# Optimization experiments

Measured on AMD Instinct MI355X. Metric: run time of the kernel, lower is better.

## Reference

```python
import jax, jax.numpy as jnp
import numpy as np

B, T, E = 8, 2048, 512   # batch, tokens, embedding_dim
K, C = 8192, 8           # num_embeddings, codebook_dim
LN_EPS = 1e-5


def _layer_norm(x, g, b):
    mu = jnp.mean(x, axis=-1, keepdims=True)
    var = jnp.var(x, axis=-1, keepdims=True)
    return (x - mu) * jax.lax.rsqrt(var + LN_EPS) * g + b


def setup_inputs() -> dict:
    key = jax.random.key(0)
    ks = jax.random.split(key, 8)
    s_e = 1.0 / np.sqrt(E)
    s_c = 1.0 / np.sqrt(C)
    return {
        "features": jax.random.normal(ks[0], (B, T, E), dtype=jnp.float32),
        # project_in: Linear(E,E) -> ReLU -> Linear(E,C)
        "W1_in": jax.random.uniform(ks[1], (E, E), jnp.float32, -s_e, s_e),
        "b1_in": jnp.zeros((E,), jnp.float32),
        "W2_in": jax.random.uniform(ks[2], (E, C), jnp.float32, -s_e, s_e),
        "b2_in": jnp.zeros((C,), jnp.float32),
        "ln_in_g": jnp.ones((C,), jnp.float32),
        "ln_in_b": jnp.zeros((C,), jnp.float32),
        # codebook
        "emb": jax.random.normal(ks[3], (K, C), dtype=jnp.float32),
        # project_out: Linear(C,E) -> ReLU -> Linear(E,E)
        "W1_out": jax.random.uniform(ks[4], (C, E), jnp.float32, -s_c, s_c),
        "b1_out": jnp.zeros((E,), jnp.float32),
        "W2_out": jax.random.uniform(ks[5], (E, E), jnp.float32, -s_e, s_e),
        "b2_out": jnp.zeros((E,), jnp.float32),
        "ln_out_g": jnp.ones((E,), jnp.float32),
        "ln_out_b": jnp.zeros((E,), jnp.float32),
    }


def reference(features, W1_in, b1_in, W2_in, b2_in, ln_in_g, ln_in_b, emb,
              W1_out, b1_out, W2_out, b2_out, ln_out_g, ln_out_b):
    # project_in + norm_in
    h = jax.nn.relu(jnp.einsum('bte,ef->btf', features, W1_in) + b1_in)
    z = jnp.einsum('bte,ec->btc', h, W2_in) + b2_in          # (B,T,C)
    z = _layer_norm(z, ln_in_g, ln_in_b)
    zf = z.reshape(-1, C)                                     # (N,C)
    d = (jnp.sum(zf * zf, axis=1, keepdims=True)
         - 2.0 * zf @ emb.T
         + jnp.sum(emb * emb, axis=1)[None, :])               # (N,K)
    idx = jnp.argmin(d, axis=1)                               # (N,)
    encodings = jax.nn.one_hot(idx, K, dtype=zf.dtype)        # (N,K)
    quantized = emb[idx]                                      # gather == one_hot @ emb
    # project_out + norm_out
    q = jax.nn.relu(quantized @ W1_out + b1_out)
    q = q @ W2_out + b2_out
    q = _layer_norm(q, ln_out_g, ln_out_b)
    q = q.reshape(B, T, E)
    return q, idx[:, None], encodings
```

## Files before the change

### kernel.cpp

```cpp
#include <hip/hip_runtime.h>
#include <cstdint>
#include <cstddef>

#define N_TOK 16384
#define E_DIM 512
#define C_DIM 8
#define K_CODES 8192
#define LN_EPS 1e-5f

typedef __attribute__((ext_vector_type(8))) short short8;
typedef __attribute__((ext_vector_type(4))) float f32x4;

__device__ __forceinline__ unsigned short bf16_rn(float x) {
  unsigned u = __float_as_uint(x);
  unsigned r = u + 0x7FFFu + ((u >> 16) & 1u);
  return (unsigned short)(r >> 16);
}
__device__ __forceinline__ float bf16_f(unsigned short h) {
  return __uint_as_float(((unsigned)h) << 16);
}

__device__ __forceinline__ void gload16(const void* g, void* l) {
  __builtin_amdgcn_global_load_lds(
      (const __attribute__((address_space(1))) void*)g,
      (__attribute__((address_space(3))) void*)l, 16, 0, 0);
}

__device__ __forceinline__ void pack_a_body(const float* __restrict__ A,
    unsigned short* __restrict__ hi, unsigned short* __restrict__ lo, int t) {
  int l = t & 63;
  int kt = (t >> 6) & 15;
  int mf = t >> 10;
  const float* src = A + (size_t)(mf * 16 + (l & 15)) * 512 + kt * 32 + (l >> 4) * 8;
  float4 x0 = *(const float4*)src;
  float4 x1 = *(const float4*)(src + 4);
  float xs[8] = {x0.x, x0.y, x0.z, x0.w, x1.x, x1.y, x1.z, x1.w};
  unsigned hw[4], lw[4];
#pragma unroll
  for (int p = 0; p < 4; ++p) {
    float a = xs[2 * p], b = xs[2 * p + 1];
    unsigned short ha = bf16_rn(a), hb = bf16_rn(b);
    unsigned short la = bf16_rn(a - bf16_f(ha)), lb = bf16_rn(b - bf16_f(hb));
    hw[p] = (unsigned)ha | ((unsigned)hb << 16);
    lw[p] = (unsigned)la | ((unsigned)lb << 16);
  }
  uint4 hv; hv.x = hw[0]; hv.y = hw[1]; hv.z = hw[2]; hv.w = hw[3];
  uint4 lv; lv.x = lw[0]; lv.y = lw[1]; lv.z = lw[2]; lv.w = lw[3];
  ((uint4*)hi)[t] = hv;
  ((uint4*)lo)[t] = lv;
}

__device__ __forceinline__ void pack_b_body(const float* __restrict__ B,
    unsigned short* __restrict__ hi, unsigned short* __restrict__ lo, int t) {
  int l = t & 63;
  int kt = (t >> 6) & 15;
  int nf = t >> 10;
  int col = nf * 16 + (l & 15);
  int krow = kt * 32 + (l >> 4) * 8;
  unsigned hw[4], lw[4];
#pragma unroll
  for (int p = 0; p < 4; ++p) {
    float a = B[(size_t)(krow + 2 * p) * 512 + col];
    float b = B[(size_t)(krow + 2 * p + 1) * 512 + col];
    unsigned short ha = bf16_rn(a), hb = bf16_rn(b);
    unsigned short la = bf16_rn(a - bf16_f(ha)), lb = bf16_rn(b - bf16_f(hb));
    hw[p] = (unsigned)ha | ((unsigned)hb << 16);
    lw[p] = (unsigned)la | ((unsigned)lb << 16);
  }
  uint4 hv; hv.x = hw[0]; hv.y = hw[1]; hv.z = hw[2]; hv.w = hw[3];
  uint4 lv; lv.x = lw[0]; lv.y = lw[1]; lv.z = lw[2]; lv.w = lw[3];
  ((uint4*)hi)[t] = hv;
  ((uint4*)lo)[t] = lv;
}

__global__ __launch_bounds__(256) void prep(const float* __restrict__ features,
    const float* __restrict__ W1_in, const float* __restrict__ W2_out,
    const float* __restrict__ emb,
    const float* __restrict__ W1_out, const float* __restrict__ b1_out,
    unsigned short* __restrict__ A1h, unsigned short* __restrict__ A1l,
    unsigned short* __restrict__ B1h, unsigned short* __restrict__ B1l,
    unsigned short* __restrict__ B2h, unsigned short* __restrict__ B2l,
    unsigned short* __restrict__ A2h, unsigned short* __restrict__ A2l,
    float* __restrict__ ne) {
  int bid = blockIdx.x;
  int tid = threadIdx.x;
  if (bid < 4096) {
    pack_a_body(features, A1h, A1l, bid * 256 + tid);
  } else if (bid < 4224) {
    pack_b_body(W1_in, B1h, B1l, (bid - 4096) * 256 + tid);
  } else if (bid < 4352) {
    pack_b_body(W2_out, B2h, B2l, (bid - 4224) * 256 + tid);
  } else if (bid < 4384) {
    int k = (bid - 4352) * 256 + tid;
    const float* e = emb + (size_t)k * C_DIM;
    float s = 0.f;
#pragma unroll
    for (int c = 0; c < C_DIM; ++c) s = fmaf(e[c], e[c], s);
    ne[k] = s;
  } else {
    int mf = bid - 4384;
    int l = tid & 63;
    int kt4 = tid >> 6;
    int k0 = mf * 16 + (l & 15);
    float ev[C_DIM];
#pragma unroll
    for (int c = 0; c < C_DIM; ++c) ev[c] = emb[(size_t)k0 * C_DIM + c];
#pragma unroll
    for (int it = 0; it < 4; ++it) {
      int kt = it * 4 + kt4;
      int e0 = kt * 32 + (l >> 4) * 8;
      float o[8];
      float4 bv0 = *(const float4*)(b1_out + e0);
      float4 bv1 = *(const float4*)(b1_out + e0 + 4);
      o[0] = bv0.x; o[1] = bv0.y; o[2] = bv0.z; o[3] = bv0.w;
      o[4] = bv1.x; o[5] = bv1.y; o[6] = bv1.z; o[7] = bv1.w;
#pragma unroll
      for (int c = 0; c < C_DIM; ++c) {
        float4 w0 = *(const float4*)(W1_out + (size_t)c * E_DIM + e0);
        float4 w1 = *(const float4*)(W1_out + (size_t)c * E_DIM + e0 + 4);
        o[0] = fmaf(ev[c], w0.x, o[0]); o[1] = fmaf(ev[c], w0.y, o[1]);
        o[2] = fmaf(ev[c], w0.z, o[2]); o[3] = fmaf(ev[c], w0.w, o[3]);
        o[4] = fmaf(ev[c], w1.x, o[4]); o[5] = fmaf(ev[c], w1.y, o[5]);
        o[6] = fmaf(ev[c], w1.z, o[6]); o[7] = fmaf(ev[c], w1.w, o[7]);
      }
      unsigned hw[4], lw[4];
#pragma unroll
      for (int p = 0; p < 4; ++p) {
        float a = fmaxf(o[2 * p], 0.f), b = fmaxf(o[2 * p + 1], 0.f);
        unsigned short ha = bf16_rn(a), hb = bf16_rn(b);
        unsigned short la = bf16_rn(a - bf16_f(ha)), lb = bf16_rn(b - bf16_f(hb));
        hw[p] = (unsigned)ha | ((unsigned)hb << 16);
        lw[p] = (unsigned)la | ((unsigned)lb << 16);
      }
      size_t t = ((size_t)mf * 16 + kt) * 64 + l;
      uint4 hv; hv.x = hw[0]; hv.y = hw[1]; hv.z = hw[2]; hv.w = hw[3];
      uint4 lv; lv.x = lw[0]; lv.y = lw[1]; lv.z = lw[2]; lv.w = lw[3];
      ((uint4*)A2h)[t] = hv;
      ((uint4*)A2l)[t] = lv;
    }
  }
}

template<bool RELU>
__global__ __launch_bounds__(256) void gemm_mfma(const unsigned short* __restrict__ Ah,
    const unsigned short* __restrict__ Al, const unsigned short* __restrict__ Bh,
    const unsigned short* __restrict__ Bl, const float* __restrict__ bias,
    float* __restrict__ C) {
  __shared__ char smem[65536];
  const int tid = threadIdx.x;
  const int l = tid & 63;
  const int w = tid >> 6;
  const int wm = w >> 1, wn = w & 1;
  const int mblk = blockIdx.y, nblk = blockIdx.x;

  const char* gAh = (const char*)Ah + (((size_t)(mblk * 8 + 2 * w) * 16) * 64 + l) * 16;
  const char* gAl = (const char*)Al + (((size_t)(mblk * 8 + 2 * w) * 16) * 64 + l) * 16;
  const char* gBh = (const char*)Bh + (((size_t)(nblk * 8 + 2 * w) * 16) * 64 + l) * 16;
  const char* gBl = (const char*)Bl + (((size_t)(nblk * 8 + 2 * w) * 16) * 64 + l) * 16;

  f32x4 acc[4][4];
#pragma unroll
  for (int i = 0; i < 4; ++i)
#pragma unroll
    for (int j = 0; j < 4; ++j) acc[i][j] = (f32x4){0.f, 0.f, 0.f, 0.f};

  auto stage = [&](int buf, int kt) {
    char* base = smem + buf * 32768;
    const size_t ko = (size_t)kt * 1024;
    char* dA0 = base + (2 * w) * 1024;
    char* dA1 = base + 8192 + (2 * w) * 1024;
    char* dB0 = base + 16384 + (2 * w) * 1024;
    char* dB1 = base + 24576 + (2 * w) * 1024;
    gload16(gAh + ko,         dA0);
    gload16(gAh + ko + 16384, dA0 + 1024);
    gload16(gAl + ko,         dA1);
    gload16(gAl + ko + 16384, dA1 + 1024);
    gload16(gBh + ko,         dB0);
    gload16(gBh + ko + 16384, dB0 + 1024);
    gload16(gBl + ko,         dB1);
    gload16(gBl + ko + 16384, dB1 + 1024);
  };

  auto compute = [&](int buf) {
    const char* base = smem + buf * 32768;
    const short8* sAh = (const short8*)(base);
    const short8* sAl = (const short8*)(base + 8192);
    const short8* sBh = (const short8*)(base + 16384);
    const short8* sBl = (const short8*)(base + 24576);
    short8 a_h[4], a_l[4], b_h[4], b_l[4];
#pragma unroll
    for (int i = 0; i < 4; ++i) {
      a_h[i] = sAh[(wm * 4 + i) * 64 + l];
      a_l[i] = sAl[(wm * 4 + i) * 64 + l];
    }
#pragma unroll
    for (int j = 0; j < 4; ++j) {
      b_h[j] = sBh[(wn * 4 + j) * 64 + l];
      b_l[j] = sBl[(wn * 4 + j) * 64 + l];
    }
#pragma unroll
    for (int i = 0; i < 4; ++i)
#pragma unroll
      for (int j = 0; j < 4; ++j)
        acc[i][j] = __builtin_amdgcn_mfma_f32_16x16x32_bf16(a_h[i], b_h[j], acc[i][j], 0, 0, 0);
#pragma unroll
    for (int i = 0; i < 4; ++i)
#pragma unroll
      for (int j = 0; j < 4; ++j)
        acc[i][j] = __builtin_amdgcn_mfma_f32_16x16x32_bf16(a_h[i], b_l[j], acc[i][j], 0, 0, 0);
#pragma unroll
    for (int i = 0; i < 4; ++i)
#pragma unroll
      for (int j = 0; j < 4; ++j)
        acc[i][j] = __builtin_amdgcn_mfma_f32_16x16x32_bf16(a_l[i], b_h[j], acc[i][j], 0, 0, 0);
  };

  stage(0, 0);
  __syncthreads();
  int cur = 0;
#pragma unroll 1
  for (int kt = 1; kt < 16; ++kt) {
    stage(cur ^ 1, kt);
    compute(cur);
    __syncthreads();
    cur ^= 1;
  }
  compute(cur);

  const int colb = nblk * 128 + wn * 64 + (l & 15);
  const int rowb = mblk * 128 + wm * 64 + ((l >> 4) << 2);
#pragma unroll
  for (int j = 0; j < 4; ++j) {
    float bv = bias[colb + j * 16];
#pragma unroll
    for (int i = 0; i < 4; ++i) {
#pragma unroll
      for (int r = 0; r < 4; ++r) {
        float v = acc[i][j][r] + bv;
        if (RELU) v = fmaxf(v, 0.f);
        C[(size_t)(rowb + i * 16 + r) * 512 + colb + j * 16] = v;
      }
    }
  }
}

__global__ __launch_bounds__(256) void zln_kernel(const float* __restrict__ h,
    const float* __restrict__ W2, const float* __restrict__ b2,
    const float* __restrict__ g, const float* __restrict__ b,
    float* __restrict__ z) {
  int token = blockIdx.x * 4 + (threadIdx.x >> 6);
  int lane = threadIdx.x & 63;
  const float* hr = h + (size_t)token * E_DIM;
  float acc[C_DIM];
#pragma unroll
  for (int c = 0; c < C_DIM; ++c) acc[c] = 0.f;
  for (int e = lane; e < E_DIM; e += 64) {
    float hv = hr[e];
    const float* w = W2 + e * C_DIM;
#pragma unroll
    for (int c = 0; c < C_DIM; ++c) acc[c] = fmaf(hv, w[c], acc[c]);
  }
#pragma unroll
  for (int c = 0; c < C_DIM; ++c) {
#pragma unroll
    for (int off = 32; off > 0; off >>= 1) acc[c] += __shfl_down(acc[c], off);
  }
  if (lane == 0) {
    float v[C_DIM]; float mu = 0.f;
#pragma unroll
    for (int c = 0; c < C_DIM; ++c) { v[c] = acc[c] + b2[c]; mu += v[c]; }
    mu *= 0.125f;
    float var = 0.f;
#pragma unroll
    for (int c = 0; c < C_DIM; ++c) { float d = v[c] - mu; var += d * d; }
    var *= 0.125f;
    float inv = 1.0f / sqrtf(var + LN_EPS);
#pragma unroll
    for (int c = 0; c < C_DIM; ++c)
      z[(size_t)token * C_DIM + c] = ((v[c] - mu) * inv) * g[c] + b[c];
  }
}

__global__ __launch_bounds__(256) void vq_partial(const float* __restrict__ z,
    const float* __restrict__ emb, const float* __restrict__ ne,
    float* __restrict__ pbest, int* __restrict__ pidx) {
  int chunk = blockIdx.x & 7;
  int token = (blockIdx.x >> 3) * 256 + threadIdx.x;
  float zv[C_DIM];
#pragma unroll
  for (int c = 0; c < C_DIM; ++c) zv[c] = z[(size_t)token * C_DIM + c];
  float s = 0.f;
#pragma unroll
  for (int c = 0; c < C_DIM; ++c) s = fmaf(zv[c], zv[c], s);
  float best = 3.402823466e38f; int bi = 0;
  int j0 = chunk * 1024;
  for (int j = j0; j < j0 + 1024; ++j) {
    const float* e = emb + (size_t)j * C_DIM;
    float p = 0.f;
#pragma unroll
    for (int c = 0; c < C_DIM; ++c) p = fmaf(zv[c], e[c], p);
    float d = fmaf(-2.f, p, s) + ne[j];
    if (d < best) { best = d; bi = j; }
  }
  pbest[chunk * N_TOK + token] = best;
  pidx[chunk * N_TOK + token] = bi;
}

__global__ void vq_combine(const float* __restrict__ pbest, const int* __restrict__ pidx,
    int* __restrict__ idx_i, float* __restrict__ idxf) {
  int n = blockIdx.x * 256 + threadIdx.x;
  float best = pbest[n]; int bi = pidx[n];
#pragma unroll
  for (int c = 1; c < 8; ++c) {
    float bb = pbest[c * N_TOK + n]; int i2 = pidx[c * N_TOK + n];
    if (bb < best) { best = bb; bi = i2; }
  }
  idx_i[n] = bi;
  idxf[n] = (float)bi;
}

__global__ __launch_bounds__(128) void gather_ln(const float* __restrict__ oc,
    const int* __restrict__ idx_i, const float* __restrict__ gw,
    const float* __restrict__ bw, float* __restrict__ q) {
  int n = blockIdx.x;
  int tid = threadIdx.x;
  int k = idx_i[n];
  const float* r = oc + (size_t)k * E_DIM;
  float4 v = ((const float4*)r)[tid];
  __shared__ float red[4];
  int lane = tid & 63, wid = tid >> 6;
  float sum = v.x + v.y + v.z + v.w;
#pragma unroll
  for (int off = 32; off > 0; off >>= 1) sum += __shfl_xor(sum, off);
  if (lane == 0) red[wid] = sum;
  __syncthreads();
  float mu = (red[0] + red[1]) * (1.0f / 512.0f);
  float4 d;
  d.x = v.x - mu; d.y = v.y - mu; d.z = v.z - mu; d.w = v.w - mu;
  float sq = d.x * d.x + d.y * d.y + d.z * d.z + d.w * d.w;
#pragma unroll
  for (int off = 32; off > 0; off >>= 1) sq += __shfl_xor(sq, off);
  if (lane == 0) red[2 + wid] = sq;
  __syncthreads();
  float var = (red[2] + red[3]) * (1.0f / 512.0f);
  float inv = 1.0f / sqrtf(var + LN_EPS);
  float4 gg = ((const float4*)gw)[tid];
  float4 bb = ((const float4*)bw)[tid];
  float4 o;
  o.x = d.x * inv * gg.x + bb.x;
  o.y = d.y * inv * gg.y + bb.y;
  o.z = d.z * inv * gg.z + bb.z;
  o.w = d.w * inv * gg.w + bb.w;
  ((float4*)(q + (size_t)n * E_DIM))[tid] = o;
}

__global__ __launch_bounds__(256) void zero_scatter(const float* __restrict__ idxf,
    float* __restrict__ enc) {
  int n = blockIdx.x;
  int tid = threadIdx.x;
  int k = (int)idxf[n];
  float* row = enc + (size_t)n * K_CODES;
  float4 zv = {0.f, 0.f, 0.f, 0.f};
#pragma unroll
  for (int u = 0; u < 8; ++u)
    ((float4*)row)[u * 256 + tid] = zv;
  if (((k >> 2) & 255) == tid) row[k] = 1.0f;
}

extern "C" void kernel_launch(void* const* d_in, const int* in_sizes, int n_in,
                              void* d_out, int out_size, void* d_ws, size_t ws_size,
                              hipStream_t stream) {
  const float* features = (const float*)d_in[0];
  const float* W1_in  = (const float*)d_in[1];
  const float* b1_in  = (const float*)d_in[2];
  const float* W2_in  = (const float*)d_in[3];
  const float* b2_in  = (const float*)d_in[4];
  const float* ln_in_g = (const float*)d_in[5];
  const float* ln_in_b = (const float*)d_in[6];
  const float* emb    = (const float*)d_in[7];
  const float* W1_out = (const float*)d_in[8];
  const float* b1_out = (const float*)d_in[9];
  const float* W2_out = (const float*)d_in[10];
  const float* b2_out = (const float*)d_in[11];
  const float* ln_out_g = (const float*)d_in[12];
  const float* ln_out_b = (const float*)d_in[13];

  float* q    = (float*)d_out;
  float* idxf = q + (size_t)N_TOK * E_DIM;
  float* enc  = idxf + N_TOK;

  float* h     = enc;
  float* g     = enc + 12582912;
  float* z     = enc + 16777216;
  float* ne    = enc + 16908288;
  float* pbest = enc + 16916480;
  int*   idx_i = (int*)(enc + 17047552);
  int*   pidx  = (int*)(enc + 17063936);
  unsigned short* A1h = (unsigned short*)(enc + 17195008);
  unsigned short* A1l = (unsigned short*)(enc + 21389312);
  unsigned short* A2h = (unsigned short*)(enc + 25583616);
  unsigned short* A2l = (unsigned short*)(enc + 27680768);
  unsigned short* B1h = (unsigned short*)(enc + 29777920);
  unsigned short* B1l = (unsigned short*)(enc + 29908992);
  unsigned short* B2h = (unsigned short*)(enc + 30040064);
  unsigned short* B2l = (unsigned short*)(enc + 30171136);

  prep<<<4896, 256, 0, stream>>>(features, W1_in, W2_out, emb, W1_out, b1_out,
                                 A1h, A1l, B1h, B1l, B2h, B2l, A2h, A2l, ne);

  dim3 g1(4, N_TOK / 128);
  gemm_mfma<true><<<g1, 256, 0, stream>>>(A1h, A1l, B1h, B1l, b1_in, h);

  zln_kernel<<<N_TOK / 4, 256, 0, stream>>>(h, W2_in, b2_in, ln_in_g, ln_in_b, z);

  vq_partial<<<(N_TOK / 256) * 8, 256, 0, stream>>>(z, emb, ne, pbest, pidx);
  vq_combine<<<N_TOK / 256, 256, 0, stream>>>(pbest, pidx, idx_i, idxf);

  dim3 g2(4, K_CODES / 128);
  gemm_mfma<false><<<g2, 256, 0, stream>>>(A2h, A2l, B2h, B2l, b2_out, g);

  gather_ln<<<N_TOK, 128, 0, stream>>>(g, idx_i, ln_out_g, ln_out_b, q);

  zero_scatter<<<N_TOK, 256, 0, stream>>>(idxf, enc);
}
```

Measured before the change: 781.7 us.

## Overlap one-hot zeroing with GEMM and VQ kernels, fuse combine into gather

Moves scratch buffers into the workspace when it is large enough. The one-hot encoding buffer can then be zero-filled in chunks inside the two GEMM kernels and the VQ search loop, which hides the large memset behind compute. The partial-argmin combine is fused into gather_ln, which also writes the index and plants the 1.0 entry, so vq_combine and zero_scatter no longer run. The cost is extra store traffic inside compute kernels and a dependence on workspace size.

```diff
diff --git a/kernel.cpp b/kernel.cpp
--- a/kernel.cpp
+++ b/kernel.cpp
@@ -145,7 +145,7 @@
 __global__ __launch_bounds__(256) void gemm_mfma(const unsigned short* __restrict__ Ah,
     const unsigned short* __restrict__ Al, const unsigned short* __restrict__ Bh,
     const unsigned short* __restrict__ Bl, const float* __restrict__ bias,
-    float* __restrict__ C) {
+    float* __restrict__ C, float4* __restrict__ zb) {
   __shared__ char smem[65536];
   const int tid = threadIdx.x;
   const int l = tid & 63;
@@ -157,6 +157,8 @@
   const char* gAl = (const char*)Al + (((size_t)(mblk * 8 + 2 * w) * 16) * 64 + l) * 16;
   const char* gBh = (const char*)Bh + (((size_t)(nblk * 8 + 2 * w) * 16) * 64 + l) * 16;
   const char* gBl = (const char*)Bl + (((size_t)(nblk * 8 + 2 * w) * 16) * 64 + l) * 16;
+
+  const size_t zbase = (size_t)(blockIdx.y * gridDim.x + blockIdx.x) * 32768 + tid;
 
   f32x4 acc[4][4];
 #pragma unroll
@@ -181,6 +183,15 @@
     gload16(gBl + ko + 16384, dB1 + 1024);
   };
 
+  auto zchunk = [&](int c) {
+    if (zb) {
+      float4 zv = {0.f, 0.f, 0.f, 0.f};
+      float4* dst = zb + zbase + (size_t)c * 2048;
+#pragma unroll
+      for (int u = 0; u < 8; ++u) dst[u * 256] = zv;
+    }
+  };
+
   auto compute = [&](int buf) {
     const char* base = smem + buf * 32768;
     const short8* sAh = (const short8*)(base);
@@ -216,11 +227,13 @@
   };
 
   stage(0, 0);
+  zchunk(0);
   __syncthreads();
   int cur = 0;
 #pragma unroll 1
   for (int kt = 1; kt < 16; ++kt) {
     stage(cur ^ 1, kt);
+    zchunk(kt);
     compute(cur);
     __syncthreads();
     cur ^= 1;
@@ -283,7 +296,7 @@
 
 __global__ __launch_bounds__(256) void vq_partial(const float* __restrict__ z,
     const float* __restrict__ emb, const float* __restrict__ ne,
-    float* __restrict__ pbest, int* __restrict__ pidx) {
+    float* __restrict__ pbest, int* __restrict__ pidx, float4* __restrict__ zb) {
   int chunk = blockIdx.x & 7;
   int token = (blockIdx.x >> 3) * 256 + threadIdx.x;
   float zv[C_DIM];
@@ -294,37 +307,38 @@
   for (int c = 0; c < C_DIM; ++c) s = fmaf(zv[c], zv[c], s);
   float best = 3.402823466e38f; int bi = 0;
   int j0 = chunk * 1024;
-  for (int j = j0; j < j0 + 1024; ++j) {
-    const float* e = emb + (size_t)j * C_DIM;
-    float p = 0.f;
-#pragma unroll
-    for (int c = 0; c < C_DIM; ++c) p = fmaf(zv[c], e[c], p);
-    float d = fmaf(-2.f, p, s) + ne[j];
-    if (d < best) { best = d; bi = j; }
+  const size_t zbase = (size_t)blockIdx.x * 16384 + threadIdx.x;
+  float4 z4 = {0.f, 0.f, 0.f, 0.f};
+#pragma unroll 1
+  for (int jo = 0; jo < 64; ++jo) {
+    if (zb) zb[zbase + (size_t)jo * 256] = z4;
+#pragma unroll
+    for (int ji = 0; ji < 16; ++ji) {
+      int j = j0 + jo * 16 + ji;
+      const float* e = emb + (size_t)j * C_DIM;
+      float p = 0.f;
+#pragma unroll
+      for (int c = 0; c < C_DIM; ++c) p = fmaf(zv[c], e[c], p);
+      float d = fmaf(-2.f, p, s) + ne[j];
+      if (d < best) { best = d; bi = j; }
+    }
   }
   pbest[chunk * N_TOK + token] = best;
   pidx[chunk * N_TOK + token] = bi;
 }
 
-__global__ void vq_combine(const float* __restrict__ pbest, const int* __restrict__ pidx,
-    int* __restrict__ idx_i, float* __restrict__ idxf) {
-  int n = blockIdx.x * 256 + threadIdx.x;
-  float best = pbest[n]; int bi = pidx[n];
+__global__ __launch_bounds__(128) void gather_ln(const float* __restrict__ oc,
+    const float* __restrict__ pbest, const int* __restrict__ pidx,
+    const float* __restrict__ gw, const float* __restrict__ bw,
+    float* __restrict__ q, float* __restrict__ idxf, float* __restrict__ enc_plant) {
+  int n = blockIdx.x;
+  int tid = threadIdx.x;
+  float best = pbest[n]; int k = pidx[n];
 #pragma unroll
   for (int c = 1; c < 8; ++c) {
     float bb = pbest[c * N_TOK + n]; int i2 = pidx[c * N_TOK + n];
-    if (bb < best) { best = bb; bi = i2; }
-  }
-  idx_i[n] = bi;
-  idxf[n] = (float)bi;
-}
-
-__global__ __launch_bounds__(128) void gather_ln(const float* __restrict__ oc,
-    const int* __restrict__ idx_i, const float* __restrict__ gw,
-    const float* __restrict__ bw, float* __restrict__ q) {
-  int n = blockIdx.x;
-  int tid = threadIdx.x;
-  int k = idx_i[n];
+    if (bb < best) { best = bb; k = i2; }
+  }
   const float* r = oc + (size_t)k * E_DIM;
   float4 v = ((const float4*)r)[tid];
   __shared__ float red[4];
@@ -352,6 +366,10 @@
   o.z = d.z * inv * gg.z + bb.z;
   o.w = d.w * inv * gg.w + bb.w;
   ((float4*)(q + (size_t)n * E_DIM))[tid] = o;
+  if (tid == 0) {
+    idxf[n] = (float)k;
+    if (enc_plant) enc_plant[(size_t)n * K_CODES + k] = 1.0f;
+  }
 }
 
 __global__ __launch_bounds__(256) void zero_scatter(const float* __restrict__ idxf,
@@ -389,37 +407,67 @@
   float* idxf = q + (size_t)N_TOK * E_DIM;
   float* enc  = idxf + N_TOK;
 
-  float* h     = enc;
-  float* g     = enc + 12582912;
-  float* z     = enc + 16777216;
-  float* ne    = enc + 16908288;
-  float* pbest = enc + 16916480;
-  int*   idx_i = (int*)(enc + 17047552);
-  int*   pidx  = (int*)(enc + 17063936);
-  unsigned short* A1h = (unsigned short*)(enc + 17195008);
-  unsigned short* A1l = (unsigned short*)(enc + 21389312);
-  unsigned short* A2h = (unsigned short*)(enc + 25583616);
-  unsigned short* A2l = (unsigned short*)(enc + 27680768);
-  unsigned short* B1h = (unsigned short*)(enc + 29777920);
-  unsigned short* B1l = (unsigned short*)(enc + 29908992);
-  unsigned short* B2h = (unsigned short*)(enc + 30040064);
-  unsigned short* B2l = (unsigned short*)(enc + 30171136);
+  const size_t WS_NEED = 26091520ULL * 4ULL;
+  const bool use_ws = (d_ws != nullptr) && (ws_size >= WS_NEED);
+
+  float *h, *g, *z, *ne, *pbest; int* pidx;
+  unsigned short *A1h, *A1l, *A2h, *A2l, *B1h, *B1l, *B2h, *B2l;
+  if (use_ws) {
+    float* ws = (float*)d_ws;
+    h     = ws;
+    g     = ws + 8388608;
+    z     = ws + 12582912;
+    ne    = ws + 12713984;
+    pbest = ws + 12722176;
+    pidx  = (int*)(ws + 12853248);
+    A1h = (unsigned short*)(ws + 12984320);
+    A1l = (unsigned short*)(ws + 17178624);
+    A2h = (unsigned short*)(ws + 21372928);
+    A2l = (unsigned short*)(ws + 23470080);
+    B1h = (unsigned short*)(ws + 25567232);
+    B1l = (unsigned short*)(ws + 25698304);
+    B2h = (unsigned short*)(ws + 25829376);
+    B2l = (unsigned short*)(ws + 25960448);
+  } else {
+    h     = enc;
+    g     = enc + 12582912;
+    z     = enc + 16777216;
+    ne    = enc + 16908288;
+    pbest = enc + 16916480;
+    pidx  = (int*)(enc + 17063936);
+    A1h = (unsigned short*)(enc + 17195008);
+    A1l = (unsigned short*)(enc + 21389312);
+    A2h = (unsigned short*)(enc + 25583616);
+    A2l = (unsigned short*)(enc + 27680768);
+    B1h = (unsigned short*)(enc + 29777920);
+    B1l = (unsigned short*)(enc + 29908992);
+    B2h = (unsigned short*)(enc + 30040064);
+    B2l = (unsigned short*)(enc + 30171136);
+  }
+
+  float4* encv = (float4*)enc;
+  float4* zb1 = use_ws ? encv            : nullptr;
+  float4* zb2 = use_ws ? encv + 16777216 : nullptr;
+  float4* zbv = use_ws ? encv + 25165824 : nullptr;
+  float*  plant = use_ws ? enc : nullptr;
 
   prep<<<4896, 256, 0, stream>>>(features, W1_in, W2_out, emb, W1_out, b1_out,
                                  A1h, A1l, B1h, B1l, B2h, B2l, A2h, A2l, ne);
 
   dim3 g1(4, N_TOK / 128);
-  gemm_mfma<true><<<g1, 256, 0, stream>>>(A1h, A1l, B1h, B1l, b1_in, h);
+  gemm_mfma<true><<<g1, 256, 0, stream>>>(A1h, A1l, B1h, B1l, b1_in, h, zb1);
 
   zln_kernel<<<N_TOK / 4, 256, 0, stream>>>(h, W2_in, b2_in, ln_in_g, ln_in_b, z);
 
-  vq_partial<<<(N_TOK / 256) * 8, 256, 0, stream>>>(z, emb, ne, pbest, pidx);
-  vq_combine<<<N_TOK / 256, 256, 0, stream>>>(pbest, pidx, idx_i, idxf);
+  vq_partial<<<(N_TOK / 256) * 8, 256, 0, stream>>>(z, emb, ne, pbest, pidx, zbv);
 
   dim3 g2(4, K_CODES / 128);
-  gemm_mfma<false><<<g2, 256, 0, stream>>>(A2h, A2l, B2h, B2l, b2_out, g);
-
-  gather_ln<<<N_TOK, 128, 0, stream>>>(g, idx_i, ln_out_g, ln_out_b, q);
-
-  zero_scatter<<<N_TOK, 256, 0, stream>>>(idxf, enc);
-}
+  gemm_mfma<false><<<g2, 256, 0, stream>>>(A2h, A2l, B2h, B2l, b2_out, g, zb2);
+
+  gather_ln<<<N_TOK, 128, 0, stream>>>(g, pbest, pidx, ln_out_g, ln_out_b,
+                                       q, idxf, plant);
+
+  if (!use_ws) {
+    zero_scatter<<<N_TOK, 256, 0, stream>>>(idxf, enc);
+  }
+}
```

Result: slower. 882.6 us (+12.9%).
